# Optimization experiments

Measured on AMD Instinct MI355X. Metric: run time of the kernel, lower is better.

Reference implementation:

```python
import jax, jax.numpy as jnp
import numpy as np

# Fixed supermask = [3, 4, 16, 28, 0, 0, 0, 3]:
#   preproc: relu(Linear x3); l1 = GCN(x); l2 = GCN(l1); l3 = GCN(l2);
#   out = relu(Linear z3((l1+l2+l3)/3))
HIDDEN = 64


def gcn_conv(h, W, b, src, dst, norm, n_nodes):
    # PyG GCNConv: h' = scatter_add(norm * (hW)[src] -> dst) + b
    hw = h @ W                                  # [N, F]
    msg = hw[src] * norm[:, None]               # gather + scale  [E+N, F]
    agg = jax.ops.segment_sum(msg, dst, num_segments=n_nodes)
    return agg + b


def setup_inputs() -> dict:
    key = jax.random.key(0)
    ks = jax.random.split(key, 12)
    N, E, NFEAT, NCLASS = 100000, 1000000, 256, 40
    x = jax.random.normal(ks[0], (N, NFEAT), dtype=jnp.float32)
    edge_index = jax.random.randint(ks[1], (2, E), 0, N, dtype=jnp.int64)
    s = 1.0 / np.sqrt(NFEAT)
    h = 1.0 / np.sqrt(HIDDEN)
    return {
        "x": x,
        "edge_index": edge_index,
        "Wx": jax.random.uniform(ks[2], (NFEAT, HIDDEN), jnp.float32, -s, s),
        "bx": jnp.zeros((HIDDEN,), jnp.float32),
        "W1": jax.random.uniform(ks[3], (HIDDEN, HIDDEN), jnp.float32, -h, h),
        "b1": jnp.zeros((HIDDEN,), jnp.float32),
        "W2": jax.random.uniform(ks[4], (HIDDEN, HIDDEN), jnp.float32, -h, h),
        "b2": jnp.zeros((HIDDEN,), jnp.float32),
        "W3": jax.random.uniform(ks[5], (HIDDEN, HIDDEN), jnp.float32, -h, h),
        "b3": jnp.zeros((HIDDEN,), jnp.float32),
        "Wz": jax.random.uniform(ks[6], (HIDDEN, NCLASS), jnp.float32, -h, h),
        "bz": jnp.zeros((NCLASS,), jnp.float32),
    }


def reference(x, edge_index, Wx, bx, W1, b1, W2, b2, W3, b3, Wz, bz):
    n = x.shape[0]
    # add self-loops (PyG GCNConv default)
    loop = jnp.arange(n, dtype=edge_index.dtype)
    src = jnp.concatenate([edge_index[0], loop])
    dst = jnp.concatenate([edge_index[1], loop])
    deg = jax.ops.segment_sum(jnp.ones_like(dst, dtype=x.dtype), dst, num_segments=n)
    dinv = jnp.where(deg > 0, jax.lax.rsqrt(deg), 0.0)
    norm = dinv[src] * dinv[dst]                 # [E+N]

    h0 = jax.nn.relu(x @ Wx + bx)                # x_3(relu) o x3(Linear)
    l1 = gcn_conv(h0, W1, b1, src, dst, norm, n)
    l2 = gcn_conv(l1, W2, b2, src, dst, norm, n)
    l3 = gcn_conv(l2, W3, b3, src, dst, norm, n)
    z = (l1 + l2 + l3) / 3.0
    return jax.nn.relu(z @ Wz + bz)
```

## Files before the change

kernel.cpp:

```cpp
#include <hip/hip_runtime.h>

#define NFEAT 256
#define HID 64
#define NCLASS 40
#define EPB 4096
#define BCAP 8192

typedef _Float16 half8 __attribute__((ext_vector_type(8)));
typedef float floatx4 __attribute__((ext_vector_type(4)));

__global__ __launch_bounds__(256) void k_bin(const int* __restrict__ src, const int* __restrict__ dst,
                                             int* __restrict__ bcur, int* __restrict__ bwords,
                                             int nbuckets, int E) {
    __shared__ int lcnt[256], loff[256], lcur[256], gbase[256], sc[256];
    __shared__ int sdst[EPB];
    __shared__ int words[EPB];
    int t = threadIdx.x;
    int base = blockIdx.x * EPB;
    int n = E - base; if (n > EPB) n = EPB;
    lcnt[t] = 0;
    __syncthreads();
    for (int i = t; i < n; i += 256) {
        int d = dst[base + i];
        sdst[i] = d;
        atomicAdd(&lcnt[d >> 9], 1);
    }
    __syncthreads();
    int v = lcnt[t];
    sc[t] = v; __syncthreads();
    for (int o = 1; o < 256; o <<= 1) {
        int add = (t >= o) ? sc[t - o] : 0;
        __syncthreads();
        sc[t] += add;
        __syncthreads();
    }
    int excl = sc[t] - v;
    loff[t] = excl; lcur[t] = excl;
    __syncthreads();
    for (int i = t; i < n; i += 256) {
        int d = sdst[i], s = src[base + i];
        int b = d >> 9;
        int p = atomicAdd(&lcur[b], 1);
        words[p] = s | ((d & 511) << 17);
    }
    __syncthreads();
    if (t < nbuckets) {
        int c = lcnt[t];
        gbase[t] = c > 0 ? atomicAdd(&bcur[t], c) : 0;
    }
    __syncthreads();
    int lane = t & 63, wv = t >> 6;
    for (int b = wv; b < nbuckets; b += 4) {
        int o = loff[b], c = lcnt[b], gb = gbase[b];
        int* dstp = bwords + (size_t)b * BCAP;
        for (int i = lane; i < c; i += 64) {
            int gp = gb + i;
            if (gp < BCAP) dstp[gp] = words[o + i];
        }
    }
}

__global__ __launch_bounds__(256) void k_csr(const int* __restrict__ bcur, const int* __restrict__ bwords,
                                             int* __restrict__ csr, unsigned* __restrict__ pk,
                                             float* __restrict__ dinv, int N) {
    __shared__ int cnt[512], cur[512], sc[256];
    __shared__ int lcsr[BCAP];
    int t = threadIdx.x;
    int b = blockIdx.x;
    int nodebase = b << 9;
    int nb = bcur[b]; if (nb > BCAP) nb = BCAP;
    cnt[t] = 0; cnt[t + 256] = 0;
    __syncthreads();
    const int* wp = bwords + (size_t)b * BCAP;
    for (int i = t; i < nb; i += 256)
        atomicAdd(&cnt[wp[i] >> 17], 1);
    __syncthreads();
    int v0 = cnt[2 * t], v1 = cnt[2 * t + 1];
    int p = v0 + v1;
    sc[t] = p; __syncthreads();
    for (int o = 1; o < 256; o <<= 1) {
        int add = (t >= o) ? sc[t - o] : 0;
        __syncthreads();
        sc[t] += add;
        __syncthreads();
    }
    int e = sc[t] - p;
    cur[2 * t] = e; cur[2 * t + 1] = e + v0;
    #pragma unroll
    for (int j = 0; j < 2; ++j) {
        int node = nodebase + 2 * t + j;
        if (node < N) {
            int c = cnt[2 * t + j]; if (c > 2047) c = 2047;
            pk[node] = (unsigned)(b * BCAP + cur[2 * t + j]) | ((unsigned)c << 21);
            dinv[node] = rsqrtf((float)c + 1.0f);
        }
    }
    __syncthreads();
    for (int i = t; i < nb; i += 256) {
        int w = wp[i];
        int pos = atomicAdd(&cur[w >> 17], 1);
        lcsr[pos] = w & 0x1FFFF;
    }
    __syncthreads();
    int* cp = csr + (size_t)b * BCAP;
    for (int i = t; i < nb; i += 256) cp[i] = lcsr[i];
}

__global__ __launch_bounds__(512) void k_gemm_in(const float* __restrict__ x, const float* __restrict__ Wx,
                                                 const float* __restrict__ bx, _Float16* __restrict__ h0, int N) {
    __shared__ _Float16 Wt[64][264];
    int t = threadIdx.x;
    {
        int c = t & 63, k0 = (t >> 6) * 32;
        for (int k = k0; k < k0 + 32; ++k)
            Wt[c][k] = (_Float16)Wx[k * HID + c];
    }
    __syncthreads();
    int lane = t & 63, lg = lane >> 4, ln = lane & 15;
    int wid = (blockIdx.x * 512 + t) >> 6;
    int nw = (gridDim.x * 512) >> 6;
    float bb[4];
    #pragma unroll
    for (int g = 0; g < 4; ++g) bb[g] = bx[g * 16 + ln];
    int ntiles = N >> 4;
    for (int tile = wid; tile < ntiles; tile += nw) {
        int row0 = tile << 4;
        const float* xr = x + (size_t)(row0 + ln) * NFEAT + lg * 8;
        float4 av[16];
        #pragma unroll
        for (int ks = 0; ks < 8; ++ks) {
            av[2 * ks]     = *(const float4*)(xr + ks * 32);
            av[2 * ks + 1] = *(const float4*)(xr + ks * 32 + 4);
        }
        floatx4 acc[4] = {{0.f,0.f,0.f,0.f},{0.f,0.f,0.f,0.f},{0.f,0.f,0.f,0.f},{0.f,0.f,0.f,0.f}};
        #pragma unroll
        for (int ks = 0; ks < 8; ++ks) {
            float4 a0 = av[2 * ks], a1 = av[2 * ks + 1];
            half8 a;
            a[0]=(_Float16)a0.x; a[1]=(_Float16)a0.y; a[2]=(_Float16)a0.z; a[3]=(_Float16)a0.w;
            a[4]=(_Float16)a1.x; a[5]=(_Float16)a1.y; a[6]=(_Float16)a1.z; a[7]=(_Float16)a1.w;
            #pragma unroll
            for (int g = 0; g < 4; ++g) {
                half8 b = *(const half8*)&Wt[g * 16 + ln][ks * 32 + lg * 8];
                acc[g] = __builtin_amdgcn_mfma_f32_16x16x32_f16(a, b, acc[g], 0, 0, 0);
            }
        }
        #pragma unroll
        for (int g = 0; g < 4; ++g) {
            #pragma unroll
            for (int r = 0; r < 4; ++r) {
                int row = row0 + lg * 4 + r;
                h0[(size_t)row * HID + g * 16 + ln] = (_Float16)fmaxf(acc[g][r] + bb[g], 0.f);
            }
        }
    }
}

__global__ __launch_bounds__(256) void k_layer(const _Float16* __restrict__ Ph, const int* __restrict__ csr,
                                               const unsigned* __restrict__ pk, const float* __restrict__ dinv,
                                               const float* __restrict__ W, const float* __restrict__ b,
                                               _Float16* __restrict__ Lout, int N) {
    __shared__ _Float16 z[32][72];
    __shared__ _Float16 ot[32][72];
    int t = threadIdx.x;
    int lane = t & 63, wv = t >> 6;
    int sg = lane >> 3, f8 = lane & 7;
    int lg = lane >> 4, ln = lane & 15;
    int nb = blockIdx.x << 5;
    half8 bf[2];
    #pragma unroll
    for (int ks = 0; ks < 2; ++ks)
        #pragma unroll
        for (int j = 0; j < 8; ++j)
            bf[ks][j] = (_Float16)W[(ks * 32 + lg * 8 + j) * HID + wv * 16 + ln];
    float bb = b[wv * 16 + ln];
    int node = nb + wv * 8 + sg;
    if (node < N) {
        unsigned pkv = pk[node];
        int off = (int)(pkv & 0x1FFFFFu);
        int c = (int)(pkv >> 21);
        float dd = dinv[node];
        half8 self = *(const half8*)(Ph + (size_t)node * HID + f8 * 8);
        float dd2 = dd * dd;
        float acc[8];
        #pragma unroll
        for (int j = 0; j < 8; ++j) acc[j] = (float)self[j] * dd2;
        for (int jj = 0; jj < c; jj += 8) {
            int e = jj + f8;
            bool ok = e < c;
            int s = ok ? csr[off + e] : 0;
            float nm = ok ? dinv[s] * dd : 0.f;
            #pragma unroll
            for (int k = 0; k < 8; ++k) {
                int ss = __shfl(s, k, 8);
                float nn = __shfl(nm, k, 8);
                half8 v = *(const half8*)(Ph + (size_t)ss * HID + f8 * 8);
                #pragma unroll
                for (int j = 0; j < 8; ++j) acc[j] += (float)v[j] * nn;
            }
        }
        half8 zv;
        #pragma unroll
        for (int j = 0; j < 8; ++j) zv[j] = (_Float16)acc[j];
        *(half8*)&z[wv * 8 + sg][f8 * 8] = zv;
    }
    __syncthreads();
    floatx4 acc0 = {0.f, 0.f, 0.f, 0.f}, acc1 = {0.f, 0.f, 0.f, 0.f};
    #pragma unroll
    for (int ks = 0; ks < 2; ++ks) {
        half8 a0 = *(const half8*)&z[ln][ks * 32 + lg * 8];
        half8 a1 = *(const half8*)&z[16 + ln][ks * 32 + lg * 8];
        acc0 = __builtin_amdgcn_mfma_f32_16x16x32_f16(a0, bf[ks], acc0, 0, 0, 0);
        acc1 = __builtin_amdgcn_mfma_f32_16x16x32_f16(a1, bf[ks], acc1, 0, 0, 0);
    }
    #pragma unroll
    for (int r = 0; r < 4; ++r) {
        ot[lg * 4 + r][wv * 16 + ln] = (_Float16)(acc0[r] + bb);
        ot[16 + lg * 4 + r][wv * 16 + ln] = (_Float16)(acc1[r] + bb);
    }
    __syncthreads();
    {
        int row = t >> 3, c8 = t & 7;
        int onode = nb + row;
        if (onode < N)
            *(half8*)(Lout + (size_t)onode * HID + c8 * 8) = *(const half8*)&ot[row][c8 * 8];
    }
}

__global__ __launch_bounds__(256) void k_gemm_out(const _Float16* __restrict__ L1, const _Float16* __restrict__ L2,
                                                  const _Float16* __restrict__ L3, const float* __restrict__ Wz,
                                                  const float* __restrict__ bz, float* __restrict__ outp, int N) {
    int t = threadIdx.x;
    int lane = t & 63, lg = lane >> 4, ln = lane & 15;
    int wid = (blockIdx.x * 256 + t) >> 6;
    int nw = (gridDim.x * 256) >> 6;
    half8 b[2][3];
    float bb[3];
    #pragma unroll
    for (int g = 0; g < 3; ++g) {
        int col = g * 16 + ln;
        bb[g] = (col < NCLASS) ? bz[col] : 0.f;
        #pragma unroll
        for (int ks = 0; ks < 2; ++ks)
            #pragma unroll
            for (int j = 0; j < 8; ++j)
                b[ks][g][j] = (col < NCLASS) ? (_Float16)(Wz[(ks * 32 + lg * 8 + j) * NCLASS + col] * (1.f / 3.f)) : (_Float16)0.f;
    }
    int ntiles = N >> 4;
    for (int tile = wid; tile < ntiles; tile += nw) {
        int row0 = tile << 4;
        size_t rb = (size_t)(row0 + ln) * HID + lg * 8;
        floatx4 acc[3] = {{0.f,0.f,0.f,0.f},{0.f,0.f,0.f,0.f},{0.f,0.f,0.f,0.f}};
        #pragma unroll
        for (int ks = 0; ks < 2; ++ks) {
            half8 a1 = *(const half8*)(L1 + rb + ks * 32);
            half8 a2 = *(const half8*)(L2 + rb + ks * 32);
            half8 a3 = *(const half8*)(L3 + rb + ks * 32);
            half8 a;
            #pragma unroll
            for (int j = 0; j < 8; ++j)
                a[j] = (_Float16)((float)a1[j] + (float)a2[j] + (float)a3[j]);
            #pragma unroll
            for (int g = 0; g < 3; ++g)
                acc[g] = __builtin_amdgcn_mfma_f32_16x16x32_f16(a, b[ks][g], acc[g], 0, 0, 0);
        }
        #pragma unroll
        for (int g = 0; g < 3; ++g) {
            int col = g * 16 + ln;
            if (col < NCLASS) {
                #pragma unroll
                for (int r = 0; r < 4; ++r)
                    outp[(size_t)(row0 + lg * 4 + r) * NCLASS + col] = fmaxf(acc[g][r] + bb[g], 0.f);
            }
        }
    }
}

extern "C" void kernel_launch(void* const* d_in, const int* in_sizes, int n_in,
                              void* d_out, int out_size, void* d_ws, size_t ws_size,
                              hipStream_t stream) {
    const float* x  = (const float*)d_in[0];
    const int*   ei = (const int*)d_in[1];
    const float* Wx = (const float*)d_in[2];
    const float* bx = (const float*)d_in[3];
    const float* W1 = (const float*)d_in[4];
    const float* b1 = (const float*)d_in[5];
    const float* W2 = (const float*)d_in[6];
    const float* b2 = (const float*)d_in[7];
    const float* W3 = (const float*)d_in[8];
    const float* b3 = (const float*)d_in[9];
    const float* Wz = (const float*)d_in[10];
    const float* bz = (const float*)d_in[11];
    float* out = (float*)d_out;

    int N = in_sizes[0] / NFEAT;
    int E = in_sizes[1] / 2;
    const int* src = ei;
    const int* dst = ei + E;
    int nbuckets = (N + 511) >> 9;

    size_t nh = (size_t)N * HID;
    size_t Npad = ((size_t)N + 7) / 8 * 8;
    int*      bcur = (int*)d_ws;
    float*    dinv = (float*)d_ws + 256;
    unsigned* pk   = (unsigned*)(dinv + Npad);
    _Float16* H0   = (_Float16*)(pk + Npad);
    _Float16* L1   = H0 + nh;
    _Float16* L2   = L1 + nh;
    _Float16* L3   = L2 + nh;
    int*      bwords = (int*)(L3 + nh);
    int*      csr  = bwords + (size_t)nbuckets * BCAP;

    hipMemsetAsync(bcur, 0, 256 * sizeof(int), stream);
    k_bin<<<(E + EPB - 1) / EPB, 256, 0, stream>>>(src, dst, bcur, bwords, nbuckets, E);
    k_csr<<<nbuckets, 256, 0, stream>>>(bcur, bwords, csr, pk, dinv, N);

    k_gemm_in<<<256, 512, 0, stream>>>(x, Wx, bx, H0, N);

    const _Float16* Hin[3]  = {H0, L1, L2};
    _Float16*       Lout[3] = {L1, L2, L3};
    const float* Wl[3] = {W1, W2, W3};
    const float* bl[3] = {b1, b2, b3};
    int layer_blocks = (N + 31) / 32;
    for (int l = 0; l < 3; ++l)
        k_layer<<<layer_blocks, 256, 0, stream>>>(Hin[l], csr, pk, dinv, Wl[l], bl[l], Lout[l], N);

    k_gemm_out<<<512, 256, 0, stream>>>(L1, L2, L3, Wz, bz, out, N);
}
```

Measured before the change: 314.8 us.

## Stage neighbor gathers via global_load_lds, cache edge norms, pretranspose weights

The layer kernel now gathers neighbor feature rows with direct global-to-LDS loads into a per-wave staging buffer, waiting once per batch of eight edges instead of issuing register gathers. The first layer writes per-edge normalization values to a buffer that later layers read back, which avoids the dependent dinv[src] gather. Layer weights are converted to fp16 and transposed once inside extra blocks of the binning kernel, so each layer loads them as vectors. The trade-offs are extra LDS use, which may lower occupancy, a full vmcnt wait per batch, and wave-uniform loop trip counts that make shorter rows in a wave idle.

```diff
diff --git a/kernel.cpp b/kernel.cpp
--- a/kernel.cpp
+++ b/kernel.cpp
@@ -9,13 +9,31 @@
 typedef _Float16 half8 __attribute__((ext_vector_type(8)));
 typedef float floatx4 __attribute__((ext_vector_type(4)));
 
+__device__ __forceinline__ void gld_lds16(const _Float16* g, _Float16* l) {
+    __builtin_amdgcn_global_load_lds(
+        (const __attribute__((address_space(1))) void*)g,
+        (__attribute__((address_space(3))) void*)l, 16, 0, 0);
+}
+
 __global__ __launch_bounds__(256) void k_bin(const int* __restrict__ src, const int* __restrict__ dst,
                                              int* __restrict__ bcur, int* __restrict__ bwords,
-                                             int nbuckets, int E) {
+                                             int nbuckets, int E, int nbin,
+                                             const float* __restrict__ W1, const float* __restrict__ W2,
+                                             const float* __restrict__ W3, _Float16* __restrict__ Wt16) {
     __shared__ int lcnt[256], loff[256], lcur[256], gbase[256], sc[256];
     __shared__ int sdst[EPB];
     __shared__ int words[EPB];
     int t = threadIdx.x;
+    if (blockIdx.x >= (unsigned)nbin) {
+        int l = blockIdx.x - nbin;
+        const float* Ws = (l == 0) ? W1 : (l == 1) ? W2 : W3;
+        _Float16* wt = Wt16 + l * 4096;
+        for (int i = t; i < 4096; i += 256) {
+            int col = i >> 6, k = i & 63;
+            wt[i] = (_Float16)Ws[k * HID + col];
+        }
+        return;
+    }
     int base = blockIdx.x * EPB;
     int n = E - base; if (n > EPB) n = EPB;
     lcnt[t] = 0;
@@ -156,49 +174,71 @@
     }
 }
 
+template<int WRN>
 __global__ __launch_bounds__(256) void k_layer(const _Float16* __restrict__ Ph, const int* __restrict__ csr,
                                                const unsigned* __restrict__ pk, const float* __restrict__ dinv,
-                                               const float* __restrict__ W, const float* __restrict__ b,
+                                               const _Float16* __restrict__ Wt, const float* __restrict__ b,
+                                               float* __restrict__ normf,
                                                _Float16* __restrict__ Lout, int N) {
+    __shared__ _Float16 stage[4][8][8][64];
     __shared__ _Float16 z[32][72];
-    __shared__ _Float16 ot[32][72];
+    _Float16 (*ot)[72] = (_Float16 (*)[72])&stage[0][0][0][0];
     int t = threadIdx.x;
     int lane = t & 63, wv = t >> 6;
     int sg = lane >> 3, f8 = lane & 7;
     int lg = lane >> 4, ln = lane & 15;
     int nb = blockIdx.x << 5;
-    half8 bf[2];
-    #pragma unroll
-    for (int ks = 0; ks < 2; ++ks)
-        #pragma unroll
-        for (int j = 0; j < 8; ++j)
-            bf[ks][j] = (_Float16)W[(ks * 32 + lg * 8 + j) * HID + wv * 16 + ln];
-    float bb = b[wv * 16 + ln];
     int node = nb + wv * 8 + sg;
-    if (node < N) {
-        unsigned pkv = pk[node];
-        int off = (int)(pkv & 0x1FFFFFu);
-        int c = (int)(pkv >> 21);
-        float dd = dinv[node];
-        half8 self = *(const half8*)(Ph + (size_t)node * HID + f8 * 8);
+    int nodec = node < N ? node : (N - 1);
+    int col = wv * 16 + ln;
+    half8 bf0 = *(const half8*)(Wt + col * 64 + lg * 8);
+    half8 bf1 = *(const half8*)(Wt + col * 64 + 32 + lg * 8);
+    float bb = b[col];
+
+    unsigned pkv = (node < N) ? pk[node] : 0u;
+    int off = (int)(pkv & 0x1FFFFFu);
+    int c = (int)(pkv >> 21);
+    float dd = (node < N) ? dinv[node] : 0.f;
+    float acc[8];
+    {
+        half8 self = *(const half8*)(Ph + (size_t)nodec * HID + f8 * 8);
         float dd2 = dd * dd;
-        float acc[8];
         #pragma unroll
         for (int j = 0; j < 8; ++j) acc[j] = (float)self[j] * dd2;
-        for (int jj = 0; jj < c; jj += 8) {
-            int e = jj + f8;
-            bool ok = e < c;
-            int s = ok ? csr[off + e] : 0;
-            float nm = ok ? dinv[s] * dd : 0.f;
-            #pragma unroll
-            for (int k = 0; k < 8; ++k) {
-                int ss = __shfl(s, k, 8);
-                float nn = __shfl(nm, k, 8);
-                half8 v = *(const half8*)(Ph + (size_t)ss * HID + f8 * 8);
-                #pragma unroll
-                for (int j = 0; j < 8; ++j) acc[j] += (float)v[j] * nn;
+    }
+    int cm = c;
+    cm = max(cm, __shfl_xor(cm, 8));
+    cm = max(cm, __shfl_xor(cm, 16));
+    cm = max(cm, __shfl_xor(cm, 32));
+    for (int jj = 0; jj < cm; jj += 8) {
+        int e = jj + f8;
+        bool ok = e < c;
+        int s = nodec;
+        float nm = 0.f;
+        if (ok) {
+            s = csr[off + e];
+            if (WRN) {
+                nm = dinv[s] * dd;
+                normf[off + e] = nm;
+            } else {
+                nm = normf[off + e];
             }
         }
+        #pragma unroll
+        for (int j = 0; j < 8; ++j) {
+            int ss = __shfl(s, j, 8);
+            gld_lds16(Ph + (size_t)ss * HID + f8 * 8, &stage[wv][j][0][0]);
+        }
+        asm volatile("s_waitcnt vmcnt(0)" ::: "memory");
+        #pragma unroll
+        for (int j = 0; j < 8; ++j) {
+            float nn = __shfl(nm, j, 8);
+            half8 v = *(const half8*)&stage[wv][j][sg][f8 * 8];
+            #pragma unroll
+            for (int q = 0; q < 8; ++q) acc[q] = fmaf((float)v[q], nn, acc[q]);
+        }
+    }
+    {
         half8 zv;
         #pragma unroll
         for (int j = 0; j < 8; ++j) zv[j] = (_Float16)acc[j];
@@ -206,12 +246,15 @@
     }
     __syncthreads();
     floatx4 acc0 = {0.f, 0.f, 0.f, 0.f}, acc1 = {0.f, 0.f, 0.f, 0.f};
-    #pragma unroll
-    for (int ks = 0; ks < 2; ++ks) {
-        half8 a0 = *(const half8*)&z[ln][ks * 32 + lg * 8];
-        half8 a1 = *(const half8*)&z[16 + ln][ks * 32 + lg * 8];
-        acc0 = __builtin_amdgcn_mfma_f32_16x16x32_f16(a0, bf[ks], acc0, 0, 0, 0);
-        acc1 = __builtin_amdgcn_mfma_f32_16x16x32_f16(a1, bf[ks], acc1, 0, 0, 0);
+    {
+        half8 a0 = *(const half8*)&z[ln][lg * 8];
+        half8 a1 = *(const half8*)&z[16 + ln][lg * 8];
+        acc0 = __builtin_amdgcn_mfma_f32_16x16x32_f16(a0, bf0, acc0, 0, 0, 0);
+        acc1 = __builtin_amdgcn_mfma_f32_16x16x32_f16(a1, bf0, acc1, 0, 0, 0);
+        a0 = *(const half8*)&z[ln][32 + lg * 8];
+        a1 = *(const half8*)&z[16 + ln][32 + lg * 8];
+        acc0 = __builtin_amdgcn_mfma_f32_16x16x32_f16(a0, bf1, acc0, 0, 0, 0);
+        acc1 = __builtin_amdgcn_mfma_f32_16x16x32_f16(a1, bf1, acc1, 0, 0, 0);
     }
     #pragma unroll
     for (int r = 0; r < 4; ++r) {
@@ -310,20 +353,20 @@
     _Float16* L3   = L2 + nh;
     int*      bwords = (int*)(L3 + nh);
     int*      csr  = bwords + (size_t)nbuckets * BCAP;
-
+    _Float16* Wt16 = (_Float16*)(csr + (size_t)nbuckets * BCAP);
+    float*    normf = (float*)(Wt16 + 3 * 4096);
+
+    int nbin = (E + EPB - 1) / EPB;
     hipMemsetAsync(bcur, 0, 256 * sizeof(int), stream);
-    k_bin<<<(E + EPB - 1) / EPB, 256, 0, stream>>>(src, dst, bcur, bwords, nbuckets, E);
+    k_bin<<<nbin + 3, 256, 0, stream>>>(src, dst, bcur, bwords, nbuckets, E, nbin, W1, W2, W3, Wt16);
     k_csr<<<nbuckets, 256, 0, stream>>>(bcur, bwords, csr, pk, dinv, N);
 
     k_gemm_in<<<256, 512, 0, stream>>>(x, Wx, bx, H0, N);
 
-    const _Float16* Hin[3]  = {H0, L1, L2};
-    _Float16*       Lout[3] = {L1, L2, L3};
-    const float* Wl[3] = {W1, W2, W3};
-    const float* bl[3] = {b1, b2, b3};
     int layer_blocks = (N + 31) / 32;
-    for (int l = 0; l < 3; ++l)
-        k_layer<<<layer_blocks, 256, 0, stream>>>(Hin[l], csr, pk, dinv, Wl[l], bl[l], Lout[l], N);
+    k_layer<1><<<layer_blocks, 256, 0, stream>>>(H0, csr, pk, dinv, Wt16,          b1, normf, L1, N);
+    k_layer<0><<<layer_blocks, 256, 0, stream>>>(L1, csr, pk, dinv, Wt16 + 4096,   b2, normf, L2, N);
+    k_layer<0><<<layer_blocks, 256, 0, stream>>>(L2, csr, pk, dinv, Wt16 + 8192,   b3, normf, L3, N);
 
     k_gemm_out<<<512, 256, 0, stream>>>(L1, L2, L3, Wz, bz, out, N);
 }
```

After: 333.0 us. 5.8% more time.
